# Kernel tuning notes

Hardware: AMD Instinct MI355X
Metric: run time of the kernel (lower is better)

The kernel has to match this reference:

```python
import jax, jax.numpy as jnp
import numpy as np

B, S = 32, 512  # batch, seq_len


def setup_inputs() -> dict:
    key = jax.random.key(0)
    k1, k2, k3 = jax.random.split(key, 3)
    x = jax.random.normal(k1, (B, S, S), jnp.float32)
    # W[i, q, r]: weight of Linear_{i} (out q, in r); only [:i+1,:i+1] block is live
    W = jax.random.normal(k2, (S, S, S), jnp.float32) * 0.05
    b = jax.random.normal(k3, (S, S), jnp.float32) * 0.05  # b[i, q]
    return {"x": x, "W": W, "b": b}


def reference(x, W, b):
    Sl = x.shape[1]
    ar = jnp.arange(Sl)
    # --- gather anti-diagonals: D[b, i, r] = x[b, r, i - r] for r <= i, else 0 ---
    c = ar[:, None] - ar[None, :]            # [S, S]: col index i - r
    valid = c >= 0                            # r <= i
    c_clip = jnp.clip(c, 0, Sl - 1)
    D = jnp.where(valid[None], x[:, ar[None, :], c_clip], 0.0)  # [B, S, S]
    # --- per-diagonal ragged linear, batched as one einsum ---
    # padded entries of D are 0, so garbage in W beyond the live block contributes nothing
    out = jnp.einsum('bir,iqr->biq', D, W) + b[None]  # [B, S, S]
    # --- scatter back: y[b, r, cc] = out[b, r+cc, r] if r+cc < S else x unchanged ---
    rr = ar[:, None]
    cc = ar[None, :]
    ii = rr + cc                              # anti-diagonal index of position (r, cc)
    in_range = ii < Sl
    ii_clip = jnp.minimum(ii, Sl - 1)
    rr_b = jnp.broadcast_to(rr, (Sl, Sl))
    y = jnp.where(in_range[None], out[:, ii_clip, rr_b], x)
    return y
```

## Files before the change

kernel.cpp:

```cpp
#include <hip/hip_runtime.h>
#include <hip/hip_bf16.h>
#include <stdint.h>

#define SS 512
#define BB 32
#define TQ 128

typedef __bf16 bf16;
typedef __attribute__((ext_vector_type(8))) __bf16 bf16x8;
typedef __attribute__((ext_vector_type(4))) float f32x4;

__global__ __launch_bounds__(256) void copy_x_kernel(const float* __restrict__ x,
                                                     float* __restrict__ y) {
    size_t idx = (size_t)blockIdx.x * 256 + threadIdx.x;
    reinterpret_cast<float4*>(y)[idx] = reinterpret_cast<const float4*>(x)[idx];
}

__global__ __launch_bounds__(256) void gather_kernel(const float* __restrict__ x,
                                                     uint4* __restrict__ D2) {
    const int rb = blockIdx.x;
    const int b  = blockIdx.y;
    __shared__ float xs[8][516];

    const int t = threadIdx.x;
    const float* xb = x + ((size_t)b * SS + rb * 8) * SS;
#pragma unroll
    for (int k = 0; k < 4; ++k) {
        int task = t + 256 * k;
        int c4 = task & 127;
        int e  = task >> 7;
        float4 v = *reinterpret_cast<const float4*>(xb + (size_t)e * SS + c4 * 4);
        *reinterpret_cast<float4*>(&xs[e][c4 * 4]) = v;
    }
    __syncthreads();

    const int r0 = rb * 8;
#pragma unroll
    for (int k = 0; k < 2; ++k) {
        int i = t + 256 * k;
        bf16x8 pack;
#pragma unroll
        for (int e = 0; e < 8; ++e) {
            int c  = i - (r0 + e);
            int cc = c < 0 ? 0 : c;
            float v = xs[e][cc];
            pack[e] = (c >= 0) ? (bf16)v : (bf16)0.0f;
        }
        D2[((size_t)rb * BB + b) * SS + i] = __builtin_bit_cast(uint4, pack);
    }
}

template <int WRITE_O>
__global__ __launch_bounds__(256) void mfma_gemm_kernel(const uint4* __restrict__ D2,
                                                        const float* __restrict__ W,
                                                        const float* __restrict__ bias,
                                                        float* __restrict__ out) {
    const int bid = (int)blockIdx.x;
    const int xcd = bid & 7;
    const int m   = bid >> 3;
    const int run = xcd + 8 * (m >> 3);
    const int i   = (SS - 1) - (run * 8 + (m & 7));
    const int q0  = (int)blockIdx.y * TQ;
    if (q0 > i) return;

    const int qmax = ((i >> 4) + 1) * 16;
    const int qhi  = min(qmax - q0, TQ);
    const int nk   = (i >> 5) + 1;

    __shared__ bf16 Bs[TQ][40];

    const int t    = (int)threadIdx.x;
    const int lane = t & 63;
    const int w    = t >> 6;
    const int l15  = lane & 15;
    const int lg   = lane >> 4;

    f32x4 acc[2][2];
#pragma unroll
    for (int n = 0; n < 2; ++n)
#pragma unroll
        for (int m2 = 0; m2 < 2; ++m2) acc[n][m2] = (f32x4)0.0f;

    const float* Wi  = W + (size_t)i * SS * SS;
    const uint4* D2i = D2 + i;

    for (int kk = 0; kk < nk; ++kk) {
        const int r0 = kk * 32;
        __syncthreads();

#pragma unroll
        for (int s = 0; s < 2; ++s) {
            int task = t + 256 * s;
            if (task < qhi * 4) {
                int qq = task >> 2;
                int ch = task & 3;
                const float* wp = Wi + (size_t)(q0 + qq) * SS + r0 + ch * 8;
                float4 v0 = *reinterpret_cast<const float4*>(wp);
                float4 v1 = *reinterpret_cast<const float4*>(wp + 4);
                bf16x8 pk;
                pk[0] = (bf16)v0.x; pk[1] = (bf16)v0.y; pk[2] = (bf16)v0.z; pk[3] = (bf16)v0.w;
                pk[4] = (bf16)v1.x; pk[5] = (bf16)v1.y; pk[6] = (bf16)v1.z; pk[7] = (bf16)v1.w;
                *reinterpret_cast<uint4*>(&Bs[qq][ch * 8]) = __builtin_bit_cast(uint4, pk);
            }
        }

        const uint4 a0 = D2i[(size_t)(((r0 >> 3) + lg) * BB + l15) * SS];
        const uint4 a1 = D2i[(size_t)(((r0 >> 3) + lg) * BB + 16 + l15) * SS];

        __syncthreads();

        const bf16x8 aa0 = __builtin_bit_cast(bf16x8, a0);
        const bf16x8 aa1 = __builtin_bit_cast(bf16x8, a1);
#pragma unroll
        for (int n = 0; n < 2; ++n) {
            const int f  = n * 4 + w;
            const int qf = q0 + f * 16;
            if (qf <= i) {
                uint4 bv = *reinterpret_cast<const uint4*>(&Bs[f * 16 + l15][lg * 8]);
                bf16x8 bb = __builtin_bit_cast(bf16x8, bv);
                acc[n][0] = __builtin_amdgcn_mfma_f32_16x16x32_bf16(aa0, bb, acc[n][0], 0, 0, 0);
                acc[n][1] = __builtin_amdgcn_mfma_f32_16x16x32_bf16(aa1, bb, acc[n][1], 0, 0, 0);
            }
        }
    }

#pragma unroll
    for (int n = 0; n < 2; ++n) {
        const int f  = n * 4 + w;
        const int qf = q0 + f * 16;
        if (qf <= i) {
            const int q  = qf + l15;
            const float bv = bias[(size_t)i * SS + q];
            if (WRITE_O) {
#pragma unroll
                for (int m2 = 0; m2 < 2; ++m2)
#pragma unroll
                    for (int v = 0; v < 4; ++v) {
                        const int b = m2 * 16 + lg * 4 + v;
                        out[((size_t)b * SS + i) * SS + q] = acc[n][m2][v] + bv;
                    }
            } else {
                const bool ok = (q <= i);
#pragma unroll
                for (int m2 = 0; m2 < 2; ++m2)
#pragma unroll
                    for (int v = 0; v < 4; ++v) {
                        const int b = m2 * 16 + lg * 4 + v;
                        if (ok) out[((size_t)b * SS + q) * SS + (i - q)] = acc[n][m2][v] + bv;
                    }
            }
        }
    }
}

__global__ __launch_bounds__(256) void shear_kernel(const float* __restrict__ O,
                                                    const float* __restrict__ x,
                                                    float* __restrict__ y) {
    const int c0 = (int)blockIdx.x * 64;
    const int q0 = (int)blockIdx.y * 64;
    const int b  = (int)blockIdx.z;
    const int t  = (int)threadIdx.x;
    const float* xb = x + (size_t)b * SS * SS;
    float* yb       = y + (size_t)b * SS * SS;
    const int i0 = q0 + c0;

    if (i0 >= SS) {
#pragma unroll
        for (int k = 0; k < 4; ++k) {
            int task = t + 256 * k;
            int qq = task >> 4, c4 = (task & 15) * 4;
            size_t off = (size_t)(q0 + qq) * SS + c0 + c4;
            *reinterpret_cast<float4*>(yb + off) =
                *reinterpret_cast<const float4*>(xb + off);
        }
        return;
    }

    __shared__ float Os[127 * 67];
    const int nrows = min(127, SS - i0);
    const float* Ob = O + (size_t)b * SS * SS;

    for (int task = t; task < nrows * 16; task += 256) {
        int rr = task >> 4, q4 = (task & 15) * 4;
        float4 v = *reinterpret_cast<const float4*>(Ob + (size_t)(i0 + rr) * SS + q0 + q4);
        float* d = &Os[rr * 67 + q4];
        d[0] = v.x; d[1] = v.y; d[2] = v.z; d[3] = v.w;
    }
    __syncthreads();

#pragma unroll
    for (int k = 0; k < 4; ++k) {
        int task = t + 256 * k;
        int qq = task >> 4, c4 = (task & 15) * 4;
        int q = q0 + qq, c = c0 + c4;
        float4 o;
        if (i0 + qq + c4 + 3 < SS) {
            o.x = Os[(qq + c4 + 0) * 67 + qq];
            o.y = Os[(qq + c4 + 1) * 67 + qq];
            o.z = Os[(qq + c4 + 2) * 67 + qq];
            o.w = Os[(qq + c4 + 3) * 67 + qq];
        } else {
            float tmp[4];
#pragma unroll
            for (int kk = 0; kk < 4; ++kk) {
                tmp[kk] = (q + c + kk < SS) ? Os[(qq + c4 + kk) * 67 + qq]
                                            : xb[(size_t)q * SS + c + kk];
            }
            o = make_float4(tmp[0], tmp[1], tmp[2], tmp[3]);
        }
        *reinterpret_cast<float4*>(yb + (size_t)q * SS + c) = o;
    }
}

#define FTK 32
#define FWROW (TQ + 4)
__global__ __launch_bounds__(256) void diag_gemm_fallback(const float* __restrict__ x,
                                                          const float* __restrict__ W,
                                                          const float* __restrict__ bias,
                                                          float* __restrict__ y) {
    const int i  = (SS - 1) - (int)blockIdx.y;
    const int q0 = (int)blockIdx.x * TQ;
    if (q0 > i) return;
    __shared__ float Ds[FTK][BB];
    __shared__ float Ws[FTK][FWROW];
    const int tid = (int)threadIdx.x;
    const int qg  = tid & 31;
    const int bg  = tid >> 5;
    float acc[4][4];
#pragma unroll
    for (int a = 0; a < 4; ++a)
#pragma unroll
        for (int c = 0; c < 4; ++c) acc[a][c] = 0.0f;
    const float* Wi = W + (size_t)i * SS * SS;
    for (int r0 = 0; r0 <= i; r0 += FTK) {
        __syncthreads();
        {
            const int rr = tid >> 3;
            const int b4 = (tid & 7) * 4;
            const int r  = r0 + rr;
            float4 dv = make_float4(0.f, 0.f, 0.f, 0.f);
            if (r <= i) {
                const int col = i - r;
                dv.x = x[((size_t)(b4 + 0) * SS + r) * SS + col];
                dv.y = x[((size_t)(b4 + 1) * SS + r) * SS + col];
                dv.z = x[((size_t)(b4 + 2) * SS + r) * SS + col];
                dv.w = x[((size_t)(b4 + 3) * SS + r) * SS + col];
            }
            *reinterpret_cast<float4*>(&Ds[rr][b4]) = dv;
        }
#pragma unroll
        for (int l = 0; l < 4; ++l) {
            const int idx = tid + 256 * l;
            const int qL  = idx >> 3;
            const int rc  = idx & 7;
            const int r   = r0 + rc * 4;
            const float* wp = Wi + (size_t)(q0 + qL) * SS;
            float4 wv;
            if (r + 3 < SS) {
                wv = *reinterpret_cast<const float4*>(wp + r);
            } else {
                wv.x = wp[min(r + 0, SS - 1)];
                wv.y = wp[min(r + 1, SS - 1)];
                wv.z = wp[min(r + 2, SS - 1)];
                wv.w = wp[min(r + 3, SS - 1)];
            }
            Ws[rc * 4 + 0][qL] = wv.x;
            Ws[rc * 4 + 1][qL] = wv.y;
            Ws[rc * 4 + 2][qL] = wv.z;
            Ws[rc * 4 + 3][qL] = wv.w;
        }
        __syncthreads();
#pragma unroll
        for (int rr = 0; rr < FTK; ++rr) {
            const float4 d4 = *reinterpret_cast<const float4*>(&Ds[rr][bg * 4]);
            const float4 w4 = *reinterpret_cast<const float4*>(&Ws[rr][qg * 4]);
            acc[0][0] = fmaf(d4.x, w4.x, acc[0][0]); acc[0][1] = fmaf(d4.x, w4.y, acc[0][1]);
            acc[0][2] = fmaf(d4.x, w4.z, acc[0][2]); acc[0][3] = fmaf(d4.x, w4.w, acc[0][3]);
            acc[1][0] = fmaf(d4.y, w4.x, acc[1][0]); acc[1][1] = fmaf(d4.y, w4.y, acc[1][1]);
            acc[1][2] = fmaf(d4.y, w4.z, acc[1][2]); acc[1][3] = fmaf(d4.y, w4.w, acc[1][3]);
            acc[2][0] = fmaf(d4.z, w4.x, acc[2][0]); acc[2][1] = fmaf(d4.z, w4.y, acc[2][1]);
            acc[2][2] = fmaf(d4.z, w4.z, acc[2][2]); acc[2][3] = fmaf(d4.z, w4.w, acc[2][3]);
            acc[3][0] = fmaf(d4.w, w4.x, acc[3][0]); acc[3][1] = fmaf(d4.w, w4.y, acc[3][1]);
            acc[3][2] = fmaf(d4.w, w4.z, acc[3][2]); acc[3][3] = fmaf(d4.w, w4.w, acc[3][3]);
        }
    }
    const int qb = q0 + qg * 4;
    const float4 bv = *reinterpret_cast<const float4*>(bias + (size_t)i * SS + qb);
    const float bvals[4] = {bv.x, bv.y, bv.z, bv.w};
#pragma unroll
    for (int bi = 0; bi < 4; ++bi) {
        const int b = bg * 4 + bi;
        float* yb = y + (size_t)b * SS * SS;
#pragma unroll
        for (int qi = 0; qi < 4; ++qi) {
            const int q = qb + qi;
            if (q <= i) yb[(size_t)q * SS + (i - q)] = acc[bi][qi] + bvals[qi];
        }
    }
}

extern "C" void kernel_launch(void* const* d_in, const int* in_sizes, int n_in,
                              void* d_out, int out_size, void* d_ws, size_t ws_size,
                              hipStream_t stream) {
    const float* x    = (const float*)d_in[0];
    const float* W    = (const float*)d_in[1];
    const float* bias = (const float*)d_in[2];
    float* y          = (float*)d_out;

    const size_t D2_bytes = (size_t)64 * BB * SS * 16;
    const size_t O_bytes  = (size_t)BB * SS * SS * sizeof(float);

    if (ws_size >= D2_bytes + O_bytes) {
        uint4* D2 = (uint4*)d_ws;
        float* O  = (float*)((char*)d_ws + D2_bytes);
        gather_kernel<<<dim3(64, 32), dim3(256), 0, stream>>>(x, D2);
        mfma_gemm_kernel<1><<<dim3(512, 4), dim3(256), 0, stream>>>(D2, W, bias, O);
        shear_kernel<<<dim3(8, 8, 32), dim3(256), 0, stream>>>(O, x, y);
    } else if (ws_size >= D2_bytes) {
        uint4* D2 = (uint4*)d_ws;
        copy_x_kernel<<<dim3(8192), dim3(256), 0, stream>>>(x, y);
        gather_kernel<<<dim3(64, 32), dim3(256), 0, stream>>>(x, D2);
        mfma_gemm_kernel<0><<<dim3(512, 4), dim3(256), 0, stream>>>(D2, W, bias, y);
    } else {
        copy_x_kernel<<<dim3(8192), dim3(256), 0, stream>>>(x, y);
        diag_gemm_fallback<<<dim3(SS / TQ, SS), dim3(256), 0, stream>>>(x, W, bias, y);
    }
}
```

Measured before the change: 107.9 us.

## Double-buffer W tile in LDS and prefetch next K-step into registers

```diff
diff --git a/kernel.cpp b/kernel.cpp
--- a/kernel.cpp
+++ b/kernel.cpp
@@ -67,7 +67,7 @@
     const int qhi  = min(qmax - q0, TQ);
     const int nk   = (i >> 5) + 1;
 
-    __shared__ bf16 Bs[TQ][40];
+    __shared__ bf16 Bs[2][TQ][40];
 
     const int t    = (int)threadIdx.x;
     const int lane = t & 63;
@@ -84,44 +84,78 @@
     const float* Wi  = W + (size_t)i * SS * SS;
     const uint4* D2i = D2 + i;
 
+    const int qq0 = t >> 2,          ch0 = t & 3;
+    const int qq1 = (t + 256) >> 2,  ch1 = (t + 256) & 3;
+    const bool st0 = (t < qhi * 4);
+    const bool st1 = (t + 256 < qhi * 4);
+
+    float4 w0a, w0b, w1a, w1b;
+    uint4  a0c, a1c, a0n, a1n;
+
+    auto issueW = [&](int kk) {
+        const int r0 = kk * 32;
+        if (st0) {
+            const float* wp = Wi + (size_t)(q0 + qq0) * SS + r0 + ch0 * 8;
+            w0a = *reinterpret_cast<const float4*>(wp);
+            w0b = *reinterpret_cast<const float4*>(wp + 4);
+        }
+        if (st1) {
+            const float* wp = Wi + (size_t)(q0 + qq1) * SS + r0 + ch1 * 8;
+            w1a = *reinterpret_cast<const float4*>(wp);
+            w1b = *reinterpret_cast<const float4*>(wp + 4);
+        }
+    };
+    auto issueA = [&](int kk, uint4& a0, uint4& a1) {
+        const int rb = (kk * 32) >> 3;
+        a0 = D2i[(size_t)((rb + lg) * BB + l15) * SS];
+        a1 = D2i[(size_t)((rb + lg) * BB + 16 + l15) * SS];
+    };
+    auto writeB = [&](int buf) {
+        if (st0) {
+            bf16x8 pk;
+            pk[0] = (bf16)w0a.x; pk[1] = (bf16)w0a.y; pk[2] = (bf16)w0a.z; pk[3] = (bf16)w0a.w;
+            pk[4] = (bf16)w0b.x; pk[5] = (bf16)w0b.y; pk[6] = (bf16)w0b.z; pk[7] = (bf16)w0b.w;
+            *reinterpret_cast<uint4*>(&Bs[buf][qq0][ch0 * 8]) = __builtin_bit_cast(uint4, pk);
+        }
+        if (st1) {
+            bf16x8 pk;
+            pk[0] = (bf16)w1a.x; pk[1] = (bf16)w1a.y; pk[2] = (bf16)w1a.z; pk[3] = (bf16)w1a.w;
+            pk[4] = (bf16)w1b.x; pk[5] = (bf16)w1b.y; pk[6] = (bf16)w1b.z; pk[7] = (bf16)w1b.w;
+            *reinterpret_cast<uint4*>(&Bs[buf][qq1][ch1 * 8]) = __builtin_bit_cast(uint4, pk);
+        }
+    };
+
+    issueW(0);
+    issueA(0, a0c, a1c);
+    writeB(0);
+    __syncthreads();
+
+    int cur = 0;
     for (int kk = 0; kk < nk; ++kk) {
-        const int r0 = kk * 32;
-        __syncthreads();
-
-#pragma unroll
-        for (int s = 0; s < 2; ++s) {
-            int task = t + 256 * s;
-            if (task < qhi * 4) {
-                int qq = task >> 2;
-                int ch = task & 3;
-                const float* wp = Wi + (size_t)(q0 + qq) * SS + r0 + ch * 8;
-                float4 v0 = *reinterpret_cast<const float4*>(wp);
-                float4 v1 = *reinterpret_cast<const float4*>(wp + 4);
-                bf16x8 pk;
-                pk[0] = (bf16)v0.x; pk[1] = (bf16)v0.y; pk[2] = (bf16)v0.z; pk[3] = (bf16)v0.w;
-                pk[4] = (bf16)v1.x; pk[5] = (bf16)v1.y; pk[6] = (bf16)v1.z; pk[7] = (bf16)v1.w;
-                *reinterpret_cast<uint4*>(&Bs[qq][ch * 8]) = __builtin_bit_cast(uint4, pk);
-            }
-        }
-
-        const uint4 a0 = D2i[(size_t)(((r0 >> 3) + lg) * BB + l15) * SS];
-        const uint4 a1 = D2i[(size_t)(((r0 >> 3) + lg) * BB + 16 + l15) * SS];
-
-        __syncthreads();
-
-        const bf16x8 aa0 = __builtin_bit_cast(bf16x8, a0);
-        const bf16x8 aa1 = __builtin_bit_cast(bf16x8, a1);
+        const bool more = (kk + 1 < nk);
+        if (more) {
+            issueW(kk + 1);
+            issueA(kk + 1, a0n, a1n);
+        }
+
+        const bf16x8 aa0 = __builtin_bit_cast(bf16x8, a0c);
+        const bf16x8 aa1 = __builtin_bit_cast(bf16x8, a1c);
 #pragma unroll
         for (int n = 0; n < 2; ++n) {
             const int f  = n * 4 + w;
             const int qf = q0 + f * 16;
             if (qf <= i) {
-                uint4 bv = *reinterpret_cast<const uint4*>(&Bs[f * 16 + l15][lg * 8]);
+                uint4 bv = *reinterpret_cast<const uint4*>(&Bs[cur][f * 16 + l15][lg * 8]);
                 bf16x8 bb = __builtin_bit_cast(bf16x8, bv);
                 acc[n][0] = __builtin_amdgcn_mfma_f32_16x16x32_bf16(aa0, bb, acc[n][0], 0, 0, 0);
                 acc[n][1] = __builtin_amdgcn_mfma_f32_16x16x32_bf16(aa1, bb, acc[n][1], 0, 0, 0);
             }
         }
+
+        if (more) writeB(cur ^ 1);
+        __syncthreads();
+        a0c = a0n; a1c = a1n;
+        cur ^= 1;
     }
 
 #pragma unroll
```

Measured after the change: 95.31 us. -11.7%, faster.

## Load W fragments directly into registers and double-buffer K loop

Applied to the files above, without the earlier changes.

```diff
diff --git a/kernel.cpp b/kernel.cpp
--- a/kernel.cpp
+++ b/kernel.cpp
@@ -63,11 +63,7 @@
     const int q0  = (int)blockIdx.y * TQ;
     if (q0 > i) return;
 
-    const int qmax = ((i >> 4) + 1) * 16;
-    const int qhi  = min(qmax - q0, TQ);
-    const int nk   = (i >> 5) + 1;
-
-    __shared__ bf16 Bs[TQ][40];
+    const int nk = (i >> 5) + 1;
 
     const int t    = (int)threadIdx.x;
     const int lane = t & 63;
@@ -75,6 +71,11 @@
     const int l15  = lane & 15;
     const int lg   = lane >> 4;
 
+    const int qf0 = q0 + w * 16;
+    const int qf1 = q0 + 64 + w * 16;
+    const bool v0 = (qf0 <= i);
+    const bool v1 = (qf1 <= i);
+
     f32x4 acc[2][2];
 #pragma unroll
     for (int n = 0; n < 2; ++n)
@@ -84,51 +85,65 @@
     const float* Wi  = W + (size_t)i * SS * SS;
     const uint4* D2i = D2 + i;
 
+    const size_t off0 = (size_t)(qf0 + l15) * SS + lg * 8;
+    const size_t off1 = (size_t)(qf1 + l15) * SS + lg * 8;
+
+    float4 wc0, wc1, wc2, wc3, wn0, wn1, wn2, wn3;
+    uint4  a0c, a1c, a0n, a1n;
+
+    auto loadW = [&](int r0, float4& d0, float4& d1, float4& d2, float4& d3) {
+        if (v0) {
+            d0 = *reinterpret_cast<const float4*>(Wi + off0 + r0);
+            d1 = *reinterpret_cast<const float4*>(Wi + off0 + r0 + 4);
+        }
+        if (v1) {
+            d2 = *reinterpret_cast<const float4*>(Wi + off1 + r0);
+            d3 = *reinterpret_cast<const float4*>(Wi + off1 + r0 + 4);
+        }
+    };
+    auto loadA = [&](int r0, uint4& a0, uint4& a1) {
+        const int rb = r0 >> 3;
+        a0 = D2i[(size_t)((rb + lg) * BB + l15) * SS];
+        a1 = D2i[(size_t)((rb + lg) * BB + 16 + l15) * SS];
+    };
+
+    loadW(0, wc0, wc1, wc2, wc3);
+    loadA(0, a0c, a1c);
+
     for (int kk = 0; kk < nk; ++kk) {
-        const int r0 = kk * 32;
-        __syncthreads();
-
-#pragma unroll
-        for (int s = 0; s < 2; ++s) {
-            int task = t + 256 * s;
-            if (task < qhi * 4) {
-                int qq = task >> 2;
-                int ch = task & 3;
-                const float* wp = Wi + (size_t)(q0 + qq) * SS + r0 + ch * 8;
-                float4 v0 = *reinterpret_cast<const float4*>(wp);
-                float4 v1 = *reinterpret_cast<const float4*>(wp + 4);
-                bf16x8 pk;
-                pk[0] = (bf16)v0.x; pk[1] = (bf16)v0.y; pk[2] = (bf16)v0.z; pk[3] = (bf16)v0.w;
-                pk[4] = (bf16)v1.x; pk[5] = (bf16)v1.y; pk[6] = (bf16)v1.z; pk[7] = (bf16)v1.w;
-                *reinterpret_cast<uint4*>(&Bs[qq][ch * 8]) = __builtin_bit_cast(uint4, pk);
-            }
-        }
-
-        const uint4 a0 = D2i[(size_t)(((r0 >> 3) + lg) * BB + l15) * SS];
-        const uint4 a1 = D2i[(size_t)(((r0 >> 3) + lg) * BB + 16 + l15) * SS];
-
-        __syncthreads();
-
-        const bf16x8 aa0 = __builtin_bit_cast(bf16x8, a0);
-        const bf16x8 aa1 = __builtin_bit_cast(bf16x8, a1);
-#pragma unroll
-        for (int n = 0; n < 2; ++n) {
-            const int f  = n * 4 + w;
-            const int qf = q0 + f * 16;
-            if (qf <= i) {
-                uint4 bv = *reinterpret_cast<const uint4*>(&Bs[f * 16 + l15][lg * 8]);
-                bf16x8 bb = __builtin_bit_cast(bf16x8, bv);
-                acc[n][0] = __builtin_amdgcn_mfma_f32_16x16x32_bf16(aa0, bb, acc[n][0], 0, 0, 0);
-                acc[n][1] = __builtin_amdgcn_mfma_f32_16x16x32_bf16(aa1, bb, acc[n][1], 0, 0, 0);
-            }
-        }
+        const bool more = (kk + 1 < nk);
+        if (more) {
+            loadW((kk + 1) * 32, wn0, wn1, wn2, wn3);
+            loadA((kk + 1) * 32, a0n, a1n);
+        }
+
+        const bf16x8 aa0 = __builtin_bit_cast(bf16x8, a0c);
+        const bf16x8 aa1 = __builtin_bit_cast(bf16x8, a1c);
+
+        if (v0) {
+            bf16x8 b;
+            b[0] = (bf16)wc0.x; b[1] = (bf16)wc0.y; b[2] = (bf16)wc0.z; b[3] = (bf16)wc0.w;
+            b[4] = (bf16)wc1.x; b[5] = (bf16)wc1.y; b[6] = (bf16)wc1.z; b[7] = (bf16)wc1.w;
+            acc[0][0] = __builtin_amdgcn_mfma_f32_16x16x32_bf16(aa0, b, acc[0][0], 0, 0, 0);
+            acc[0][1] = __builtin_amdgcn_mfma_f32_16x16x32_bf16(aa1, b, acc[0][1], 0, 0, 0);
+        }
+        if (v1) {
+            bf16x8 b;
+            b[0] = (bf16)wc2.x; b[1] = (bf16)wc2.y; b[2] = (bf16)wc2.z; b[3] = (bf16)wc2.w;
+            b[4] = (bf16)wc3.x; b[5] = (bf16)wc3.y; b[6] = (bf16)wc3.z; b[7] = (bf16)wc3.w;
+            acc[1][0] = __builtin_amdgcn_mfma_f32_16x16x32_bf16(aa0, b, acc[1][0], 0, 0, 0);
+            acc[1][1] = __builtin_amdgcn_mfma_f32_16x16x32_bf16(aa1, b, acc[1][1], 0, 0, 0);
+        }
+
+        wc0 = wn0; wc1 = wn1; wc2 = wn2; wc3 = wn3;
+        a0c = a0n; a1c = a1n;
     }
 
 #pragma unroll
     for (int n = 0; n < 2; ++n) {
-        const int f  = n * 4 + w;
-        const int qf = q0 + f * 16;
-        if (qf <= i) {
+        const int qf = (n == 0) ? qf0 : qf1;
+        const bool vn = (n == 0) ? v0 : v1;
+        if (vn) {
             const int q  = qf + l15;
             const float bv = bias[(size_t)i * SS + q];
             if (WRITE_O) {
```

After: 117.7 us. 1.09x slower.

## Double-buffer W tiles in diagonal GEMM and store intermediate output as bf16

Applied to the files above, without the earlier changes.

```diff
diff --git a/kernel.cpp b/kernel.cpp
--- a/kernel.cpp
+++ b/kernel.cpp
@@ -50,11 +50,10 @@
     }
 }
 
-template <int WRITE_O>
-__global__ __launch_bounds__(256) void mfma_gemm_kernel(const uint4* __restrict__ D2,
-                                                        const float* __restrict__ W,
-                                                        const float* __restrict__ bias,
-                                                        float* __restrict__ out) {
+__global__ __launch_bounds__(256) void mfma_gemm_pipe(const uint4* __restrict__ D2,
+                                                      const float* __restrict__ W,
+                                                      const float* __restrict__ bias,
+                                                      bf16* __restrict__ O) {
     const int bid = (int)blockIdx.x;
     const int xcd = bid & 7;
     const int m   = bid >> 3;
@@ -67,7 +66,7 @@
     const int qhi  = min(qmax - q0, TQ);
     const int nk   = (i >> 5) + 1;
 
-    __shared__ bf16 Bs[TQ][40];
+    __shared__ bf16 Bs[2][TQ][40];
 
     const int t    = (int)threadIdx.x;
     const int lane = t & 63;
@@ -75,85 +74,143 @@
     const int l15  = lane & 15;
     const int lg   = lane >> 4;
 
-    f32x4 acc[2][2];
-#pragma unroll
-    for (int n = 0; n < 2; ++n)
-#pragma unroll
-        for (int m2 = 0; m2 < 2; ++m2) acc[n][m2] = (f32x4)0.0f;
+    f32x4 acc00 = (f32x4)0.0f, acc01 = (f32x4)0.0f;
+    f32x4 acc10 = (f32x4)0.0f, acc11 = (f32x4)0.0f;
 
     const float* Wi  = W + (size_t)i * SS * SS;
     const uint4* D2i = D2 + i;
 
-    for (int kk = 0; kk < nk; ++kk) {
-        const int r0 = kk * 32;
-        __syncthreads();
-
-#pragma unroll
-        for (int s = 0; s < 2; ++s) {
-            int task = t + 256 * s;
-            if (task < qhi * 4) {
-                int qq = task >> 2;
-                int ch = task & 3;
-                const float* wp = Wi + (size_t)(q0 + qq) * SS + r0 + ch * 8;
-                float4 v0 = *reinterpret_cast<const float4*>(wp);
-                float4 v1 = *reinterpret_cast<const float4*>(wp + 4);
-                bf16x8 pk;
-                pk[0] = (bf16)v0.x; pk[1] = (bf16)v0.y; pk[2] = (bf16)v0.z; pk[3] = (bf16)v0.w;
-                pk[4] = (bf16)v1.x; pk[5] = (bf16)v1.y; pk[6] = (bf16)v1.z; pk[7] = (bf16)v1.w;
-                *reinterpret_cast<uint4*>(&Bs[qq][ch * 8]) = __builtin_bit_cast(uint4, pk);
-            }
-        }
-
-        const uint4 a0 = D2i[(size_t)(((r0 >> 3) + lg) * BB + l15) * SS];
-        const uint4 a1 = D2i[(size_t)(((r0 >> 3) + lg) * BB + 16 + l15) * SS];
-
-        __syncthreads();
-
-        const bf16x8 aa0 = __builtin_bit_cast(bf16x8, a0);
-        const bf16x8 aa1 = __builtin_bit_cast(bf16x8, a1);
-#pragma unroll
-        for (int n = 0; n < 2; ++n) {
-            const int f  = n * 4 + w;
-            const int qf = q0 + f * 16;
-            if (qf <= i) {
-                uint4 bv = *reinterpret_cast<const uint4*>(&Bs[f * 16 + l15][lg * 8]);
-                bf16x8 bb = __builtin_bit_cast(bf16x8, bv);
-                acc[n][0] = __builtin_amdgcn_mfma_f32_16x16x32_bf16(aa0, bb, acc[n][0], 0, 0, 0);
-                acc[n][1] = __builtin_amdgcn_mfma_f32_16x16x32_bf16(aa1, bb, acc[n][1], 0, 0, 0);
-            }
-        }
-    }
-
-#pragma unroll
-    for (int n = 0; n < 2; ++n) {
-        const int f  = n * 4 + w;
-        const int qf = q0 + f * 16;
-        if (qf <= i) {
-            const int q  = qf + l15;
-            const float bv = bias[(size_t)i * SS + q];
-            if (WRITE_O) {
-#pragma unroll
-                for (int m2 = 0; m2 < 2; ++m2)
-#pragma unroll
-                    for (int v = 0; v < 4; ++v) {
-                        const int b = m2 * 16 + lg * 4 + v;
-                        out[((size_t)b * SS + i) * SS + q] = acc[n][m2][v] + bv;
-                    }
-            } else {
-                const bool ok = (q <= i);
-#pragma unroll
-                for (int m2 = 0; m2 < 2; ++m2)
-#pragma unroll
-                    for (int v = 0; v < 4; ++v) {
-                        const int b = m2 * 16 + lg * 4 + v;
-                        if (ok) out[((size_t)b * SS + q) * SS + (i - q)] = acc[n][m2][v] + bv;
-                    }
-            }
-        }
-    }
-}
-
-__global__ __launch_bounds__(256) void shear_kernel(const float* __restrict__ O,
+    const int qq0 = t >> 2,         ch0 = t & 3;
+    const int qq1 = (t + 256) >> 2, ch1 = (t + 256) & 3;
+    const bool st0 = (t < qhi * 4);
+    const bool st1 = (t + 256 < qhi * 4);
+
+    const int qf0 = q0 + w * 16;
+    const int qf1 = q0 + 64 + w * 16;
+    const bool v0 = (qf0 <= i);
+    const bool v1 = (qf1 <= i);
+
+    float4 eW0, eW1, eW2, eW3;
+    float4 oW0, oW1, oW2, oW3;
+    uint4  eA0, eA1, oA0, oA1;
+
+#define ISSUE_W(kk, d0, d1, d2, d3)                                            \
+    do {                                                                       \
+        const int r0_ = (kk) * 32;                                             \
+        if (st0) {                                                             \
+            const float* wp_ = Wi + (size_t)(q0 + qq0) * SS + r0_ + ch0 * 8;   \
+            d0 = *reinterpret_cast<const float4*>(wp_);                        \
+            d1 = *reinterpret_cast<const float4*>(wp_ + 4);                    \
+        }                                                                      \
+        if (st1) {                                                             \
+            const float* wp_ = Wi + (size_t)(q0 + qq1) * SS + r0_ + ch1 * 8;   \
+            d2 = *reinterpret_cast<const float4*>(wp_);                        \
+            d3 = *reinterpret_cast<const float4*>(wp_ + 4);                    \
+        }                                                                      \
+    } while (0)
+
+#define ISSUE_A(kk, a0_, a1_)                                                  \
+    do {                                                                       \
+        const int rb_ = ((kk) * 32) >> 3;                                      \
+        a0_ = D2i[(size_t)((rb_ + lg) * BB + l15) * SS];                       \
+        a1_ = D2i[(size_t)((rb_ + lg) * BB + 16 + l15) * SS];                  \
+    } while (0)
+
+#define WRITE_B(buf_, d0, d1, d2, d3)                                          \
+    do {                                                                       \
+        if (st0) {                                                             \
+            bf16x8 pk_;                                                        \
+            pk_[0]=(bf16)d0.x; pk_[1]=(bf16)d0.y; pk_[2]=(bf16)d0.z; pk_[3]=(bf16)d0.w; \
+            pk_[4]=(bf16)d1.x; pk_[5]=(bf16)d1.y; pk_[6]=(bf16)d1.z; pk_[7]=(bf16)d1.w; \
+            *reinterpret_cast<uint4*>(&Bs[buf_][qq0][ch0 * 8]) = __builtin_bit_cast(uint4, pk_); \
+        }                                                                      \
+        if (st1) {                                                             \
+            bf16x8 pk_;                                                        \
+            pk_[0]=(bf16)d2.x; pk_[1]=(bf16)d2.y; pk_[2]=(bf16)d2.z; pk_[3]=(bf16)d2.w; \
+            pk_[4]=(bf16)d3.x; pk_[5]=(bf16)d3.y; pk_[6]=(bf16)d3.z; pk_[7]=(bf16)d3.w; \
+            *reinterpret_cast<uint4*>(&Bs[buf_][qq1][ch1 * 8]) = __builtin_bit_cast(uint4, pk_); \
+        }                                                                      \
+    } while (0)
+
+#define BARRIER()                                                              \
+    do {                                                                       \
+        asm volatile("s_waitcnt lgkmcnt(0)" ::: "memory");                     \
+        __builtin_amdgcn_s_barrier();                                          \
+        __builtin_amdgcn_sched_barrier(0);                                     \
+    } while (0)
+
+#define MFMA_STEP(buf_, aa0_, aa1_)                                            \
+    do {                                                                       \
+        const bf16x8 a0v_ = __builtin_bit_cast(bf16x8, aa0_);                  \
+        const bf16x8 a1v_ = __builtin_bit_cast(bf16x8, aa1_);                  \
+        if (v0) {                                                              \
+            uint4 bv_ = *reinterpret_cast<const uint4*>(&Bs[buf_][w * 16 + l15][lg * 8]); \
+            bf16x8 bb_ = __builtin_bit_cast(bf16x8, bv_);                      \
+            acc00 = __builtin_amdgcn_mfma_f32_16x16x32_bf16(a0v_, bb_, acc00, 0, 0, 0); \
+            acc01 = __builtin_amdgcn_mfma_f32_16x16x32_bf16(a1v_, bb_, acc01, 0, 0, 0); \
+        }                                                                      \
+        if (v1) {                                                              \
+            uint4 bv_ = *reinterpret_cast<const uint4*>(&Bs[buf_][64 + w * 16 + l15][lg * 8]); \
+            bf16x8 bb_ = __builtin_bit_cast(bf16x8, bv_);                      \
+            acc10 = __builtin_amdgcn_mfma_f32_16x16x32_bf16(a0v_, bb_, acc10, 0, 0, 0); \
+            acc11 = __builtin_amdgcn_mfma_f32_16x16x32_bf16(a1v_, bb_, acc11, 0, 0, 0); \
+        }                                                                      \
+    } while (0)
+
+    ISSUE_W(0, eW0, eW1, eW2, eW3);
+    ISSUE_A(0, eA0, eA1);
+    if (nk > 1) { ISSUE_W(1, oW0, oW1, oW2, oW3); ISSUE_A(1, oA0, oA1); }
+    WRITE_B(0, eW0, eW1, eW2, eW3);
+    BARRIER();
+
+    for (int kk = 0; kk < nk; kk += 2) {
+        MFMA_STEP(0, eA0, eA1);
+        if (kk + 2 < nk) {
+            ISSUE_W(kk + 2, eW0, eW1, eW2, eW3);
+            ISSUE_A(kk + 2, eA0, eA1);
+        }
+        if (kk + 1 < nk) {
+            WRITE_B(1, oW0, oW1, oW2, oW3);
+            BARRIER();
+            MFMA_STEP(1, oA0, oA1);
+            if (kk + 3 < nk) {
+                ISSUE_W(kk + 3, oW0, oW1, oW2, oW3);
+                ISSUE_A(kk + 3, oA0, oA1);
+            }
+            if (kk + 2 < nk) {
+                WRITE_B(0, eW0, eW1, eW2, eW3);
+                BARRIER();
+            }
+        }
+    }
+
+#undef ISSUE_W
+#undef ISSUE_A
+#undef WRITE_B
+#undef BARRIER
+#undef MFMA_STEP
+
+    if (v0) {
+        const int q = qf0 + l15;
+        const float bv = bias[(size_t)i * SS + q];
+#pragma unroll
+        for (int v = 0; v < 4; ++v) {
+            O[((size_t)(lg * 4 + v) * SS + i) * SS + q]      = (bf16)(acc00[v] + bv);
+            O[((size_t)(16 + lg * 4 + v) * SS + i) * SS + q] = (bf16)(acc01[v] + bv);
+        }
+    }
+    if (v1) {
+        const int q = qf1 + l15;
+        const float bv = bias[(size_t)i * SS + q];
+#pragma unroll
+        for (int v = 0; v < 4; ++v) {
+            O[((size_t)(lg * 4 + v) * SS + i) * SS + q]      = (bf16)(acc10[v] + bv);
+            O[((size_t)(16 + lg * 4 + v) * SS + i) * SS + q] = (bf16)(acc11[v] + bv);
+        }
+    }
+}
+
+__global__ __launch_bounds__(256) void shear_kernel(const bf16* __restrict__ O,
                                                     const float* __restrict__ x,
                                                     float* __restrict__ y) {
     const int c0 = (int)blockIdx.x * 64;
@@ -178,13 +235,14 @@
 
     __shared__ float Os[127 * 67];
     const int nrows = min(127, SS - i0);
-    const float* Ob = O + (size_t)b * SS * SS;
-
-    for (int task = t; task < nrows * 16; task += 256) {
-        int rr = task >> 4, q4 = (task & 15) * 4;
-        float4 v = *reinterpret_cast<const float4*>(Ob + (size_t)(i0 + rr) * SS + q0 + q4);
-        float* d = &Os[rr * 67 + q4];
-        d[0] = v.x; d[1] = v.y; d[2] = v.z; d[3] = v.w;
+    const bf16* Ob = O + (size_t)b * SS * SS;
+
+    for (int task = t; task < nrows * 8; task += 256) {
+        int rr = task >> 3, c8 = (task & 7) * 8;
+        bf16x8 v = *reinterpret_cast<const bf16x8*>(Ob + (size_t)(i0 + rr) * SS + q0 + c8);
+        float* d = &Os[rr * 67 + c8];
+#pragma unroll
+        for (int e = 0; e < 8; ++e) d[e] = (float)v[e];
     }
     __syncthreads();
 
@@ -308,19 +366,14 @@
     float* y          = (float*)d_out;
 
     const size_t D2_bytes = (size_t)64 * BB * SS * 16;
-    const size_t O_bytes  = (size_t)BB * SS * SS * sizeof(float);
+    const size_t O_bytes  = (size_t)BB * SS * SS * sizeof(bf16);
 
     if (ws_size >= D2_bytes + O_bytes) {
         uint4* D2 = (uint4*)d_ws;
-        float* O  = (float*)((char*)d_ws + D2_bytes);
+        bf16*  O  = (bf16*)((char*)d_ws + D2_bytes);
         gather_kernel<<<dim3(64, 32), dim3(256), 0, stream>>>(x, D2);
-        mfma_gemm_kernel<1><<<dim3(512, 4), dim3(256), 0, stream>>>(D2, W, bias, O);
+        mfma_gemm_pipe<<<dim3(512, 4), dim3(256), 0, stream>>>(D2, W, bias, O);
         shear_kernel<<<dim3(8, 8, 32), dim3(256), 0, stream>>>(O, x, y);
-    } else if (ws_size >= D2_bytes) {
-        uint4* D2 = (uint4*)d_ws;
-        copy_x_kernel<<<dim3(8192), dim3(256), 0, stream>>>(x, y);
-        gather_kernel<<<dim3(64, 32), dim3(256), 0, stream>>>(x, D2);
-        mfma_gemm_kernel<0><<<dim3(512, 4), dim3(256), 0, stream>>>(D2, W, bias, y);
     } else {
         copy_x_kernel<<<dim3(8192), dim3(256), 0, stream>>>(x, y);
         diag_gemm_fallback<<<dim3(SS / TQ, SS), dim3(256), 0, stream>>>(x, W, bias, y);
```

Result: faster. 92.14 us (-14.6%).
